# Optimization experiments

Measured on AMD Instinct MI355X. Metric: run time of the kernel, lower is better.

## Reference

```python
import jax, jax.numpy as jnp
import numpy as np

N_CAT = 10000   # n_categories
E = 128         # embedding_dim_c
D = 4           # n_demand
H = 128         # hidden_size
B = 32          # batch_size
S = 50          # max_session_len
I = 5000        # n_items (candidate pool)


def setup_inputs() -> dict:
    key = jax.random.key(0)
    ks = jax.random.split(key, 7)
    inp = jax.random.randint(ks[0], (B, S), 0, N_CAT)
    cand = jax.random.randint(ks[1], (I,), 0, N_CAT)
    emb_table = jax.random.normal(ks[2], (N_CAT, E), jnp.float32) * 0.02
    emb_table = emb_table.at[0].set(0.0)  # padding_idx=0
    W_demand = jax.random.normal(ks[3], (D * H, E), jnp.float32) / np.float32(np.sqrt(E))
    W_score = jax.random.normal(ks[4], (H, 2 * H), jnp.float32) / np.float32(np.sqrt(2 * H))  # torch [out,in]
    b_score = jax.random.normal(ks[5], (H,), jnp.float32) * 0.01
    w_score = jax.random.uniform(ks[6], (H,), jnp.float32, 0.0, 1.0 / np.float32(np.sqrt(H)))
    return {"input": inp, "candidate_pool_category": cand, "emb_table": emb_table,
            "W_demand": W_demand, "W_score": W_score, "b_score": b_score, "w_score": w_score}


def _forward(input, candidate_pool_category, emb_table, W_demand, W_score, b_score, w_score):
    h = w_score.shape[0]
    d = W_demand.shape[0] // h
    b, s = input.shape
    emb = emb_table[input]                                   # [B,S,E]
    hidden = (emb @ W_demand.T).reshape(b, s, d, h)          # [B,S,D,H] (hidden_key == hidden_demand)
    # demand_agg == 'exp': log(sum(exp(.), axis=seq))
    agg = jnp.log(jnp.sum(jnp.exp(hidden), axis=1))          # [B,D,H]
    # demand similarity loss: mean off-diagonal pairwise cosine similarity (batch-averaged)
    nrm = jnp.maximum(jnp.linalg.norm(agg, axis=-1, keepdims=True), 1e-8)
    u = agg / nrm
    gram = jnp.mean(jnp.einsum('bdh,beh->bde', u, u), axis=0)  # [D,D]
    off = 1.0 - jnp.eye(d, dtype=gram.dtype)
    demand_sim_loss = jnp.sum(gram * off) / (d * (d - 1))
    # split score Linear weight into demand/key halves (concat order: (agg, key))
    Wd, Wk = W_score[:, :h], W_score[:, h:]                  # each [H, H]
    agg_proj = agg @ Wd.T + b_score                          # [B,D,H]
    key_proj = jnp.einsum('bsdh,oh->bsdo', hidden, Wk)       # [B,S,D,H]
    demand_score = jnp.einsum('bsdh,h->bds',
                              jax.nn.relu(agg_proj[:, None] + key_proj), w_score)  # [B,D,S]
    cand_emb = emb_table[candidate_pool_category]            # [I,E]
    cand_hidden = (cand_emb @ W_demand.T).reshape(-1, d, h)  # [I,D,H]
    cand_proj = jnp.einsum('idh,oh->ido', cand_hidden, Wk)   # [I,D,H]
    demand_score_candidate = jnp.einsum('bdih,h->bdi',
                                        jax.nn.relu(agg_proj[:, :, None, :] + jnp.transpose(cand_proj, (1, 0, 2))[None]),
                                        w_score)             # [B,D,I]
    # score_act_fun is None -> no activation
    return demand_score, demand_score_candidate, emb, cand_emb, demand_sim_loss


def reference(input, candidate_pool_category, emb_table, W_demand, W_score, b_score, w_score):
    return _forward(input, candidate_pool_category, emb_table, W_demand, W_score, b_score, w_score)
```

## Files before the change

kernel.cpp:

```cpp
#include <hip/hip_runtime.h>

typedef __attribute__((ext_vector_type(8))) short short8;
typedef __attribute__((ext_vector_type(16))) float f32x16;

#define NROWS_IN 1600
#define NI 5000
#define BB 32
#define DDk 4
#define SS 50

__device__ __forceinline__ unsigned short f2bf(float f) {
    unsigned int u = __float_as_uint(f);
    u = (u + 0x7FFFu + ((u >> 16) & 1u)) >> 16;
    return (unsigned short)u;
}
__device__ __forceinline__ float b2f(unsigned short u) {
    return __uint_as_float(((unsigned int)u) << 16);
}

__global__ __launch_bounds__(256) void k_prep(const int* __restrict__ inp,
                                              const int* __restrict__ cand,
                                              const float* __restrict__ et,
                                              const float* __restrict__ Wd,
                                              const float* __restrict__ Ws,
                                              unsigned short* __restrict__ Wcat,
                                              unsigned short* __restrict__ Abf,
                                              float* __restrict__ o_emb,
                                              float* __restrict__ o_cemb) {
    int t = threadIdx.x;
    int blk = blockIdx.x;
    if (blk < 16) {
        const float4* src = (const float4*)Wd;
#pragma unroll
        for (int q = 0; q < 4; ++q) {
            int i = blk * 256 + t + q * 4096;
            float4 v = src[i];
            ushort4 o;
            o.x = f2bf(v.x); o.y = f2bf(v.y); o.z = f2bf(v.z); o.w = f2bf(v.w);
            *(ushort4*)(Wcat + (size_t)i * 4) = o;
        }
        return;
    }
    if (blk < 80) {
        __shared__ __align__(16) float sdw[128 * 128];
        __shared__ float wk[8][128];
        int cb = blk - 16;
        int d = cb >> 4, ot = cb & 15;
        const float4* src = (const float4*)(Wd + (size_t)d * 128 * 128);
#pragma unroll
        for (int q = 0; q < 16; ++q) {
            int i = t + q * 256;
            *(float4*)(&sdw[i * 4]) = src[i];
        }
        for (int x = t; x < 8 * 128; x += 256) {
            int ol = x >> 7, h = x & 127;
            wk[ol][h] = Ws[(ot * 8 + ol) * 256 + 128 + h];
        }
        __syncthreads();
        int e = t & 127, og = t >> 7;
        float acc[4] = {0.f, 0.f, 0.f, 0.f};
        for (int h = 0; h < 128; ++h) {
            float rd = sdw[h * 128 + e];
#pragma unroll
            for (int k = 0; k < 4; ++k) acc[k] += rd * wk[og * 4 + k][h];
        }
#pragma unroll
        for (int k = 0; k < 4; ++k) {
            int o = ot * 8 + og * 4 + k;
            Wcat[(size_t)(512 + d * 128 + o) * 128 + e] = f2bf(acc[k]);
        }
        return;
    }
    int pb = blk - 80;
    int r = pb * 8 + (t >> 5);
    int fc = t & 31;
    int id = (r < NROWS_IN) ? inp[r] : cand[r - NROWS_IN];
    float4 v = *(const float4*)(et + (size_t)id * 128 + fc * 4);
    if (r < NROWS_IN) *(float4*)(o_emb + (size_t)r * 128 + fc * 4) = v;
    else              *(float4*)(o_cemb + (size_t)(r - NROWS_IN) * 128 + fc * 4) = v;
    ushort4 o;
    o.x = f2bf(v.x); o.y = f2bf(v.y); o.z = f2bf(v.z); o.w = f2bf(v.w);
    *(ushort4*)(Abf + (size_t)r * 128 + fc * 4) = o;
}

__global__ __launch_bounds__(256) void k_gemm_in(const unsigned short* __restrict__ Abf,
                                                 const unsigned short* __restrict__ Wcat,
                                                 unsigned short* __restrict__ inhid) {
    __shared__ __align__(16) unsigned short sa[64 * 128];
    __shared__ __align__(16) unsigned short sb[128 * 128];
    int gid = blockIdx.x;
    int rt = gid >> 3, ct = gid & 7;
    int arow0 = rt * 64, wrow0 = ct * 128;
    int t = threadIdx.x;
#pragma unroll
    for (int q = 0; q < 4; ++q) {
        int x = t + q * 256;
        int r = x >> 4, ch = x & 15;
        short8 v = *(const short8*)(Abf + (size_t)(arow0 + r) * 128 + ch * 8);
        *(short8*)(sa + r * 128 + ((ch ^ (r & 15)) << 3)) = v;
    }
#pragma unroll
    for (int q = 0; q < 8; ++q) {
        int x = t + q * 256;
        int r = x >> 4, ch = x & 15;
        short8 v = *(const short8*)(Wcat + (size_t)(wrow0 + r) * 128 + ch * 8);
        *(short8*)(sb + r * 128 + ((ch ^ (r & 15)) << 3)) = v;
    }
    __syncthreads();
    int w = t >> 6, lane = t & 63;
    int rbase = (w & 1) * 32, cbase = (w >> 1) * 64;
    int lr = lane & 31, g = lane >> 5;
    int arow = rbase + lr;
    int bcol0 = cbase + lr, bcol1 = cbase + 32 + lr;
    const unsigned short* pa  = sa + arow * 128;
    const unsigned short* pb0 = sb + bcol0 * 128;
    const unsigned short* pb1 = sb + bcol1 * 128;
    int axor = arow & 15, b0x = bcol0 & 15, b1x = bcol1 & 15;
    f32x16 acc0 = {}, acc1 = {};
#pragma unroll
    for (int ks = 0; ks < 8; ++ks) {
        int chA = ks * 2 + g;
        short8 a8 = *(const short8*)(pa  + ((chA ^ axor) << 3));
        short8 b8 = *(const short8*)(pb0 + ((chA ^ b0x) << 3));
        short8 c8 = *(const short8*)(pb1 + ((chA ^ b1x) << 3));
        acc0 = __builtin_amdgcn_mfma_f32_32x32x16_bf16(a8, b8, acc0, 0, 0, 0);
        acc1 = __builtin_amdgcn_mfma_f32_32x32x16_bf16(a8, c8, acc1, 0, 0, 0);
    }
#pragma unroll
    for (int r = 0; r < 16; ++r) {
        int row_l = rbase + (r & 3) + 8 * (r >> 2) + 4 * g;
        size_t base = (size_t)(arow0 + row_l) * 1024 + wrow0;
        inhid[base + cbase + lr]      = f2bf(acc0[r]);
        inhid[base + cbase + 32 + lr] = f2bf(acc1[r]);
    }
}

__global__ __launch_bounds__(256) void k_mid(const unsigned short* __restrict__ inhid,
                                             const float* __restrict__ Ws,
                                             const float* __restrict__ bsc,
                                             const float* __restrict__ wsc,
                                             float* __restrict__ aggw,
                                             float* __restrict__ apw,
                                             float* __restrict__ o_ds) {
    __shared__ __align__(16) float sexp[2][128];
    __shared__ __align__(16) float sagg[128];
    __shared__ __align__(16) float sap[128];
    __shared__ float spart[200];
    int b = blockIdx.x >> 2, d = blockIdx.x & 3;
    int t = threadIdx.x;
    {
        int sg = t >> 7, j = t & 127;
        const unsigned short* p = inhid + (size_t)(b * SS + sg * 25) * 1024 + d * 128 + j;
        float s = 0.f;
#pragma unroll 5
        for (int si = 0; si < 25; ++si) s += expf(b2f(p[si * 1024]));
        sexp[sg][j] = s;
    }
    __syncthreads();
    if (t < 128) {
        float a = logf(sexp[0][t] + sexp[1][t]);
        sagg[t] = a;
        aggw[b * 512 + d * 128 + t] = a;
    }
    __syncthreads();
    if (t < 128) {
        const float* w = Ws + t * 256;
        float acc = bsc[t];
        for (int ch = 0; ch < 32; ++ch) {
            float4 a4 = *(const float4*)(sagg + ch * 4);
            float4 w4 = *(const float4*)(w + ch * 4);
            acc += a4.x * w4.x + a4.y * w4.y + a4.z * w4.z + a4.w * w4.w;
        }
        sap[t] = acc;
        apw[(b * DDk + d) * 128 + t] = acc;
    }
    __syncthreads();
    if (t < 200) {
        int s = t >> 2, oq = t & 3;
        const unsigned short* kpp = inhid + (size_t)(b * SS + s) * 1024 + 512 + d * 128 + oq * 32;
        float acc = 0.f;
#pragma unroll
        for (int c = 0; c < 8; ++c) {
            float4 a4 = *(const float4*)(sap + oq * 32 + c * 4);
            float4 w4 = *(const float4*)(wsc + oq * 32 + c * 4);
            ushort4 k4 = *(const ushort4*)(kpp + c * 4);
            acc += w4.x * fmaxf(a4.x + b2f(k4.x), 0.f) + w4.y * fmaxf(a4.y + b2f(k4.y), 0.f)
                 + w4.z * fmaxf(a4.z + b2f(k4.z), 0.f) + w4.w * fmaxf(a4.w + b2f(k4.w), 0.f);
        }
        spart[t] = acc;
    }
    __syncthreads();
    if (t < SS) {
        float v = spart[t * 4] + spart[t * 4 + 1] + spart[t * 4 + 2] + spart[t * 4 + 3];
        o_ds[b * (DDk * SS) + d * SS + t] = v;
    }
}

__global__ __launch_bounds__(256) void k_cand(const unsigned short* __restrict__ Abf,
                                              const unsigned short* __restrict__ Wcat,
                                              const float* __restrict__ apw,
                                              const float* __restrict__ aggw,
                                              const float* __restrict__ wsc,
                                              float* __restrict__ o_dsc,
                                              float* __restrict__ o_loss) {
    __shared__ __align__(16) char lds[66048];
    int gid = blockIdx.x;
    int t = threadIdx.x;
    if (gid >= 316) {
        float* nrm = (float*)lds;
        if (t < 128) {
            const float* a = aggw + t * 128;
            float s = 0.f;
            for (int h = 0; h < 128; ++h) s += a[h] * a[h];
            nrm[t] = fmaxf(sqrtf(s), 1e-8f);
        }
        __syncthreads();
        float lb = 0.f;
        if (t < 32) {
            const float* a = aggw + t * 512;
            float i0 = 1.f / nrm[t * 4 + 0], i1 = 1.f / nrm[t * 4 + 1];
            float i2 = 1.f / nrm[t * 4 + 2], i3 = 1.f / nrm[t * 4 + 3];
            for (int h = 0; h < 128; ++h) {
                float u0 = a[h] * i0, u1 = a[128 + h] * i1;
                float u2 = a[256 + h] * i2, u3 = a[384 + h] * i3;
                float v = u0 + u1 + u2 + u3;
                lb += v * v - (u0 * u0 + u1 * u1 + u2 * u2 + u3 * u3);
            }
        }
        for (int off = 32; off; off >>= 1) lb += __shfl_down(lb, off);
        if (t == 0) o_loss[0] = lb / (float)(BB * DDk * (DDk - 1));
        return;
    }
    unsigned short* sa  = (unsigned short*)lds;
    unsigned short* sw  = (unsigned short*)(lds + 16384);
    float*          scp = (float*)lds;
    float*          sap = (float*)(lds + 49152);
    float*          swv = (float*)(lds + 65536);

    int tile = gid >> 2, d = gid & 3;
    int i0 = tile * 64;
#pragma unroll
    for (int q = 0; q < 4; ++q) {
        int x = t + q * 256;
        int r = x >> 4, ch = x & 15;
        short8 v = {0, 0, 0, 0, 0, 0, 0, 0};
        if (i0 + r < NI) v = *(const short8*)(Abf + (size_t)(NROWS_IN + i0 + r) * 128 + ch * 8);
        *(short8*)(sa + r * 128 + ((ch ^ (r & 15)) << 3)) = v;
    }
#pragma unroll
    for (int q = 0; q < 8; ++q) {
        int x = t + q * 256;
        int r = x >> 4, ch = x & 15;
        short8 v = *(const short8*)(Wcat + (size_t)(512 + d * 128 + r) * 128 + ch * 8);
        *(short8*)(sw + r * 128 + ((ch ^ (r & 15)) << 3)) = v;
    }
    if (t < 128) swv[t] = wsc[t];
#pragma unroll
    for (int q = 0; q < 4; ++q) {
        int x = t + q * 256;
        int b = x >> 5, ch = x & 31;
        float4 v = *(const float4*)(apw + (size_t)(b * 4 + d) * 128 + ch * 4);
        *(float4*)(sap + b * 128 + ((ch ^ (b & 7)) << 2)) = v;
    }
    __syncthreads();
    int w = t >> 6, lane = t & 63;
    int rbase = (w & 1) * 32, cbase = (w >> 1) * 64;
    int lr = lane & 31, g = lane >> 5;
    int arow = rbase + lr;
    int bcol0 = cbase + lr, bcol1 = cbase + 32 + lr;
    const unsigned short* pa  = sa + arow * 128;
    const unsigned short* pb0 = sw + bcol0 * 128;
    const unsigned short* pb1 = sw + bcol1 * 128;
    int axor = arow & 15, b0x = bcol0 & 15, b1x = bcol1 & 15;
    f32x16 acc0 = {}, acc1 = {};
#pragma unroll
    for (int ks = 0; ks < 8; ++ks) {
        int chA = ks * 2 + g;
        short8 a8 = *(const short8*)(pa  + ((chA ^ axor) << 3));
        short8 b8 = *(const short8*)(pb0 + ((chA ^ b0x) << 3));
        short8 c8 = *(const short8*)(pb1 + ((chA ^ b1x) << 3));
        acc0 = __builtin_amdgcn_mfma_f32_32x32x16_bf16(a8, b8, acc0, 0, 0, 0);
        acc1 = __builtin_amdgcn_mfma_f32_32x32x16_bf16(a8, c8, acc1, 0, 0, 0);
    }
    __syncthreads();
#pragma unroll
    for (int r = 0; r < 16; ++r) {
        int row = rbase + (r & 3) + 8 * (r >> 2) + 4 * g;
        int c0 = cbase + lr, c1 = cbase + 32 + lr;
        scp[row * 128 + ((((c0 >> 2) ^ (row & 7)) << 2) | (c0 & 3))] = acc0[r];
        scp[row * 128 + ((((c1 >> 2) ^ (row & 7)) << 2) | (c1 & 3))] = acc1[r];
    }
    __syncthreads();
    int b = t >> 3, gg = t & 7;
    int bx = b & 7;
    float acc[8] = {0.f, 0.f, 0.f, 0.f, 0.f, 0.f, 0.f, 0.f};
    const float* arow2 = sap + b * 128;
    for (int ch = 0; ch < 32; ++ch) {
        float4 a4 = *(const float4*)(arow2 + ((ch ^ bx) << 2));
        float4 w4 = *(const float4*)(swv + ch * 4);
#pragma unroll
        for (int kk = 0; kk < 8; ++kk) {
            int il = kk * 8 + gg;
            float4 c4 = *(const float4*)(&scp[il * 128 + ((ch ^ (il & 7)) << 2)]);
            acc[kk] += w4.x * fmaxf(a4.x + c4.x, 0.f) + w4.y * fmaxf(a4.y + c4.y, 0.f)
                     + w4.z * fmaxf(a4.z + c4.z, 0.f) + w4.w * fmaxf(a4.w + c4.w, 0.f);
        }
    }
#pragma unroll
    for (int kk = 0; kk < 8; ++kk) {
        int i = i0 + kk * 8 + gg;
        if (i < NI) o_dsc[(size_t)b * (DDk * NI) + d * NI + i] = acc[kk];
    }
}

extern "C" void kernel_launch(void* const* d_in, const int* in_sizes, int n_in,
                              void* d_out, int out_size, void* d_ws, size_t ws_size,
                              hipStream_t stream) {
    const int*   inp  = (const int*)d_in[0];
    const int*   cand = (const int*)d_in[1];
    const float* et   = (const float*)d_in[2];
    const float* Wd   = (const float*)d_in[3];
    const float* Ws   = (const float*)d_in[4];
    const float* bsc  = (const float*)d_in[5];
    const float* wsc  = (const float*)d_in[6];

    float* out = (float*)d_out;
    float* o_ds   = out;
    float* o_dsc  = out + 6400;
    float* o_emb  = out + 646400;
    float* o_cemb = out + 851200;
    float* o_loss = out + 1491200;

    char* wsb = (char*)d_ws;
    unsigned short* Wcat  = (unsigned short*)wsb;
    unsigned short* Abf   = (unsigned short*)(wsb + 262144);
    unsigned short* inhid = (unsigned short*)(wsb + 2097152);
    float* aggw = (float*)(wsb + 2097152 + 3276800);
    float* apw  = aggw + 16384;

    hipLaunchKernelGGL(k_prep, dim3(905), dim3(256), 0, stream,
                       inp, cand, et, Wd, Ws, Wcat, Abf, o_emb, o_cemb);
    hipLaunchKernelGGL(k_gemm_in, dim3(200), dim3(256), 0, stream, Abf, Wcat, inhid);
    hipLaunchKernelGGL(k_mid, dim3(128), dim3(256), 0, stream,
                       inhid, Ws, bsc, wsc, aggw, apw, o_ds);
    hipLaunchKernelGGL(k_cand, dim3(317), dim3(256), 0, stream,
                       Abf, Wcat, apw, aggw, wsc, o_dsc, o_loss);
}
```

Baseline: 38.62 us.

## Fuse input GEMM into mid kernel, keep hidden and key projections on-chip

```diff
diff --git a/kernel.cpp b/kernel.cpp
--- a/kernel.cpp
+++ b/kernel.cpp
@@ -83,109 +83,125 @@
     *(ushort4*)(Abf + (size_t)r * 128 + fc * 4) = o;
 }
 
-__global__ __launch_bounds__(256) void k_gemm_in(const unsigned short* __restrict__ Abf,
-                                                 const unsigned short* __restrict__ Wcat,
-                                                 unsigned short* __restrict__ inhid) {
-    __shared__ __align__(16) unsigned short sa[64 * 128];
-    __shared__ __align__(16) unsigned short sb[128 * 128];
-    int gid = blockIdx.x;
-    int rt = gid >> 3, ct = gid & 7;
-    int arow0 = rt * 64, wrow0 = ct * 128;
+__global__ __launch_bounds__(256) void k_fused_mid(const unsigned short* __restrict__ Abf,
+                                                   const unsigned short* __restrict__ Wcat,
+                                                   const float* __restrict__ Ws,
+                                                   const float* __restrict__ bsc,
+                                                   const float* __restrict__ wsc,
+                                                   float* __restrict__ aggw,
+                                                   float* __restrict__ apw,
+                                                   float* __restrict__ o_ds) {
+    __shared__ __align__(16) char lds[53536];
+    unsigned short* sa   = (unsigned short*)lds;
+    unsigned short* sb   = (unsigned short*)(lds + 16384);
+    float*          skp  = (float*)lds;
+    float*          sred = (float*)(lds + 49152);
+    float*          sagg = (float*)(lds + 51712);
+    float*          sap  = (float*)(lds + 52224);
+    float*          spart= (float*)(lds + 52736);
+
+    int b = blockIdx.x >> 2, d = blockIdx.x & 3;
     int t = threadIdx.x;
 #pragma unroll
     for (int q = 0; q < 4; ++q) {
         int x = t + q * 256;
         int r = x >> 4, ch = x & 15;
-        short8 v = *(const short8*)(Abf + (size_t)(arow0 + r) * 128 + ch * 8);
+        short8 v = {0, 0, 0, 0, 0, 0, 0, 0};
+        if (r < SS) v = *(const short8*)(Abf + (size_t)(b * SS + r) * 128 + ch * 8);
         *(short8*)(sa + r * 128 + ((ch ^ (r & 15)) << 3)) = v;
     }
 #pragma unroll
     for (int q = 0; q < 8; ++q) {
         int x = t + q * 256;
         int r = x >> 4, ch = x & 15;
-        short8 v = *(const short8*)(Wcat + (size_t)(wrow0 + r) * 128 + ch * 8);
+        short8 v = *(const short8*)(Wcat + (size_t)(d * 128 + r) * 128 + ch * 8);
         *(short8*)(sb + r * 128 + ((ch ^ (r & 15)) << 3)) = v;
     }
     __syncthreads();
+
     int w = t >> 6, lane = t & 63;
-    int rbase = (w & 1) * 32, cbase = (w >> 1) * 64;
     int lr = lane & 31, g = lane >> 5;
-    int arow = rbase + lr;
-    int bcol0 = cbase + lr, bcol1 = cbase + 32 + lr;
+    int rt = w & 1, ct = w >> 1;
+    int arow = rt * 32 + lr;
+    int bcol0 = ct * 64 + lr, bcol1 = ct * 64 + 32 + lr;
     const unsigned short* pa  = sa + arow * 128;
     const unsigned short* pb0 = sb + bcol0 * 128;
     const unsigned short* pb1 = sb + bcol1 * 128;
     int axor = arow & 15, b0x = bcol0 & 15, b1x = bcol1 & 15;
-    f32x16 acc0 = {}, acc1 = {};
+    f32x16 h0 = {}, h1 = {};
 #pragma unroll
     for (int ks = 0; ks < 8; ++ks) {
         int chA = ks * 2 + g;
         short8 a8 = *(const short8*)(pa  + ((chA ^ axor) << 3));
         short8 b8 = *(const short8*)(pb0 + ((chA ^ b0x) << 3));
         short8 c8 = *(const short8*)(pb1 + ((chA ^ b1x) << 3));
-        acc0 = __builtin_amdgcn_mfma_f32_32x32x16_bf16(a8, b8, acc0, 0, 0, 0);
-        acc1 = __builtin_amdgcn_mfma_f32_32x32x16_bf16(a8, c8, acc1, 0, 0, 0);
-    }
+        h0 = __builtin_amdgcn_mfma_f32_32x32x16_bf16(a8, b8, h0, 0, 0, 0);
+        h1 = __builtin_amdgcn_mfma_f32_32x32x16_bf16(a8, c8, h1, 0, 0, 0);
+    }
+    float p0 = 0.f, p1 = 0.f;
 #pragma unroll
     for (int r = 0; r < 16; ++r) {
-        int row_l = rbase + (r & 3) + 8 * (r >> 2) + 4 * g;
-        size_t base = (size_t)(arow0 + row_l) * 1024 + wrow0;
-        inhid[base + cbase + lr]      = f2bf(acc0[r]);
-        inhid[base + cbase + 32 + lr] = f2bf(acc1[r]);
-    }
-}
-
-__global__ __launch_bounds__(256) void k_mid(const unsigned short* __restrict__ inhid,
-                                             const float* __restrict__ Ws,
-                                             const float* __restrict__ bsc,
-                                             const float* __restrict__ wsc,
-                                             float* __restrict__ aggw,
-                                             float* __restrict__ apw,
-                                             float* __restrict__ o_ds) {
-    __shared__ __align__(16) float sexp[2][128];
-    __shared__ __align__(16) float sagg[128];
-    __shared__ __align__(16) float sap[128];
-    __shared__ float spart[200];
-    int b = blockIdx.x >> 2, d = blockIdx.x & 3;
-    int t = threadIdx.x;
-    {
-        int sg = t >> 7, j = t & 127;
-        const unsigned short* p = inhid + (size_t)(b * SS + sg * 25) * 1024 + d * 128 + j;
-        float s = 0.f;
-#pragma unroll 5
-        for (int si = 0; si < 25; ++si) s += expf(b2f(p[si * 1024]));
-        sexp[sg][j] = s;
-    }
-    __syncthreads();
+        int row = rt * 32 + (r & 3) + 8 * (r >> 2) + 4 * g;
+        if (row < SS) { p0 += expf(h0[r]); p1 += expf(h1[r]); }
+    }
+    sred[bcol0 * 5 + rt * 2 + g] = p0;
+    sred[bcol1 * 5 + rt * 2 + g] = p1;
+    __syncthreads();
+#pragma unroll
+    for (int q = 0; q < 8; ++q) {
+        int x = t + q * 256;
+        int r = x >> 4, ch = x & 15;
+        short8 v = *(const short8*)(Wcat + (size_t)(512 + d * 128 + r) * 128 + ch * 8);
+        *(short8*)(sb + r * 128 + ((ch ^ (r & 15)) << 3)) = v;
+    }
     if (t < 128) {
-        float a = logf(sexp[0][t] + sexp[1][t]);
+        float s = sred[t * 5] + sred[t * 5 + 1] + sred[t * 5 + 2] + sred[t * 5 + 3];
+        float a = logf(s);
         sagg[t] = a;
         aggw[b * 512 + d * 128 + t] = a;
     }
     __syncthreads();
+    f32x16 k0 = {}, k1 = {};
+#pragma unroll
+    for (int ks = 0; ks < 8; ++ks) {
+        int chA = ks * 2 + g;
+        short8 a8 = *(const short8*)(pa  + ((chA ^ axor) << 3));
+        short8 b8 = *(const short8*)(pb0 + ((chA ^ b0x) << 3));
+        short8 c8 = *(const short8*)(pb1 + ((chA ^ b1x) << 3));
+        k0 = __builtin_amdgcn_mfma_f32_32x32x16_bf16(a8, b8, k0, 0, 0, 0);
+        k1 = __builtin_amdgcn_mfma_f32_32x32x16_bf16(a8, c8, k1, 0, 0, 0);
+    }
     if (t < 128) {
-        const float* w = Ws + t * 256;
+        const float* wr = Ws + t * 256;
         float acc = bsc[t];
         for (int ch = 0; ch < 32; ++ch) {
             float4 a4 = *(const float4*)(sagg + ch * 4);
-            float4 w4 = *(const float4*)(w + ch * 4);
+            float4 w4 = *(const float4*)(wr + ch * 4);
             acc += a4.x * w4.x + a4.y * w4.y + a4.z * w4.z + a4.w * w4.w;
         }
         sap[t] = acc;
         apw[(b * DDk + d) * 128 + t] = acc;
     }
     __syncthreads();
+#pragma unroll
+    for (int r = 0; r < 16; ++r) {
+        int row = rt * 32 + (r & 3) + 8 * (r >> 2) + 4 * g;
+        int c0 = ct * 64 + lr, c1 = ct * 64 + 32 + lr;
+        skp[row * 128 + ((((c0 >> 2) ^ (row & 7)) << 2) | (c0 & 3))] = k0[r];
+        skp[row * 128 + ((((c1 >> 2) ^ (row & 7)) << 2) | (c1 & 3))] = k1[r];
+    }
+    __syncthreads();
     if (t < 200) {
         int s = t >> 2, oq = t & 3;
-        const unsigned short* kpp = inhid + (size_t)(b * SS + s) * 1024 + 512 + d * 128 + oq * 32;
         float acc = 0.f;
 #pragma unroll
         for (int c = 0; c < 8; ++c) {
-            float4 a4 = *(const float4*)(sap + oq * 32 + c * 4);
-            float4 w4 = *(const float4*)(wsc + oq * 32 + c * 4);
-            ushort4 k4 = *(const ushort4*)(kpp + c * 4);
-            acc += w4.x * fmaxf(a4.x + b2f(k4.x), 0.f) + w4.y * fmaxf(a4.y + b2f(k4.y), 0.f)
-                 + w4.z * fmaxf(a4.z + b2f(k4.z), 0.f) + w4.w * fmaxf(a4.w + b2f(k4.w), 0.f);
+            int ch = oq * 8 + c;
+            float4 a4 = *(const float4*)(sap + ch * 4);
+            float4 w4 = *(const float4*)(wsc + ch * 4);
+            float4 k4 = *(const float4*)(&skp[s * 128 + ((ch ^ (s & 7)) << 2)]);
+            acc += w4.x * fmaxf(a4.x + k4.x, 0.f) + w4.y * fmaxf(a4.y + k4.y, 0.f)
+                 + w4.z * fmaxf(a4.z + k4.z, 0.f) + w4.w * fmaxf(a4.w + k4.w, 0.f);
         }
         spart[t] = acc;
     }
@@ -332,17 +348,15 @@
     float* o_loss = out + 1491200;
 
     char* wsb = (char*)d_ws;
-    unsigned short* Wcat  = (unsigned short*)wsb;
-    unsigned short* Abf   = (unsigned short*)(wsb + 262144);
-    unsigned short* inhid = (unsigned short*)(wsb + 2097152);
-    float* aggw = (float*)(wsb + 2097152 + 3276800);
+    unsigned short* Wcat = (unsigned short*)wsb;
+    unsigned short* Abf  = (unsigned short*)(wsb + 262144);
+    float* aggw = (float*)(wsb + 2097152);
     float* apw  = aggw + 16384;
 
     hipLaunchKernelGGL(k_prep, dim3(905), dim3(256), 0, stream,
                        inp, cand, et, Wd, Ws, Wcat, Abf, o_emb, o_cemb);
-    hipLaunchKernelGGL(k_gemm_in, dim3(200), dim3(256), 0, stream, Abf, Wcat, inhid);
-    hipLaunchKernelGGL(k_mid, dim3(128), dim3(256), 0, stream,
-                       inhid, Ws, bsc, wsc, aggw, apw, o_ds);
+    hipLaunchKernelGGL(k_fused_mid, dim3(128), dim3(256), 0, stream,
+                       Abf, Wcat, Ws, bsc, wsc, aggw, apw, o_ds);
     hipLaunchKernelGGL(k_cand, dim3(317), dim3(256), 0, stream,
                        Abf, Wcat, apw, aggw, wsc, o_dsc, o_loss);
 }
```

New measurement: 37.01 us. -4.2%, faster.
